# Kernel tuning notes

Measured on AMD Instinct MI355X. Metric: run time of the kernel, lower is better.

Reference implementation:

```python
import jax, jax.numpy as jnp
import numpy as np

N_NODES = 50000
N_EDGES = 800000
N_GRAPHS = 64
PIP = 3
N_CLASSES = 10
EPS = 1e-5


def setup_inputs() -> dict:
    key = jax.random.key(0)
    ks = jax.random.split(key, 32)
    s = 0.05
    d = {}
    d["node_feats"] = jax.random.normal(ks[0], (N_NODES, 128), jnp.float32)
    d["edge_w"] = jax.random.uniform(ks[1], (N_EDGES,), jnp.float32)
    # stacked per-branch params
    d["conv_w"] = jax.random.normal(ks[2], (PIP, 96, 128, 3), jnp.float32) * s
    d["conv_b"] = jax.random.normal(ks[3], (PIP, 96), jnp.float32) * s
    d["gcn_w"] = jax.random.normal(ks[4], (PIP, 96, 54), jnp.float32) * s
    d["gcn_b"] = jax.random.normal(ks[5], (PIP, 54), jnp.float32) * s
    d["bn1_g"] = jnp.ones((96,), jnp.float32)
    d["bn1_b"] = jnp.zeros((96,), jnp.float32)
    d["bn2_g"] = jnp.ones((54,), jnp.float32)
    d["bn2_b"] = jnp.zeros((54,), jnp.float32)
    d["bn3_g"] = jnp.ones((75,), jnp.float32)
    d["bn3_b"] = jnp.zeros((75,), jnp.float32)
    d["press_w"] = jax.random.normal(ks[6], (1, PIP, PIP), jnp.float32) * s
    d["press_b"] = jax.random.normal(ks[7], (1,), jnp.float32) * s
    d["jk_w1"] = jax.random.normal(ks[8], (54, 34), jnp.float32) * s
    d["jk_b1"] = jax.random.normal(ks[9], (34,), jnp.float32) * s
    d["jk_w2"] = jax.random.normal(ks[10], (34, 25), jnp.float32) * s
    d["jk_b2"] = jax.random.normal(ks[11], (25,), jnp.float32) * s
    d["jk_w3"] = jax.random.normal(ks[12], (25, 16), jnp.float32) * s
    d["jk_b3"] = jax.random.normal(ks[13], (16,), jnp.float32) * s
    d["cls1_w"] = jax.random.normal(ks[14], (75, 120), jnp.float32) * s
    d["cls1_b"] = jax.random.normal(ks[15], (120,), jnp.float32) * s
    d["cls2_w"] = jax.random.normal(ks[16], (120, N_CLASSES), jnp.float32) * s
    d["cls2_b"] = jax.random.normal(ks[17], (N_CLASSES,), jnp.float32) * s
    d["edge_src"] = jax.random.randint(ks[18], (N_EDGES,), 0, N_NODES)
    d["edge_dst"] = jax.random.randint(ks[19], (N_EDGES,), 0, N_NODES)
    d["graph_ids"] = jnp.sort(jax.random.randint(ks[20], (N_NODES,), 0, N_GRAPHS))
    return d


def _bn(x, g, b):
    # training-mode BatchNorm1d over axis 0
    m = x.mean(0)
    v = x.var(0)
    return g * (x - m) * jax.lax.rsqrt(v + EPS) + b


def _gconv(h, W, b, src, dst, ew, n):
    # DGL GraphConv norm='none': sum_{(u,v)} w_e * h[u] -> @W + b
    msg = h[src] * ew[:, None]              # [E, F]
    agg = jax.ops.segment_sum(msg, dst, num_segments=n)  # [N, F]
    return agg @ W + b


def _dconv1d(x, w, b, dil):
    # x: [1, Cin, N], w: [Cout, Cin, K]; 'same' length via pad=dil for K=3
    out = jax.lax.conv_general_dilated(
        x, w, window_strides=(1,), padding=[(dil, dil)],
        rhs_dilation=(dil,), dimension_numbers=('NCH', 'OIH', 'NCH'))
    return out + b[None, :, None]


def reference(node_feats, edge_w, conv_w, conv_b, gcn_w, gcn_b,
              bn1_g, bn1_b, bn2_g, bn2_b, bn3_g, bn3_b,
              press_w, press_b, jk_w1, jk_b1, jk_w2, jk_b2, jk_w3, jk_b3,
              cls1_w, cls1_b, cls2_w, cls2_b,
              edge_src, edge_dst, graph_ids):
    n = node_feats.shape[0]
    relu = jax.nn.relu
    # ---- BN_embedding ----
    h0 = node_feats.T[None]                # [1, 128, N]
    h0x = [_dconv1d(h0, conv_w[i], conv_b[i], i + 1) for i in range(PIP)]
    h2x = []
    for i in range(PIP):
        a = h0x[i % PIP][0].T              # [N, 96]
        c = h0x[(i + 1) % PIP][0].T        # [N, 96]
        h1 = _bn(relu(a) + c, bn1_g, bn1_b)          # cross_connect
        t = _gconv(h1, gcn_w[i], gcn_b[i], edge_src, edge_dst, edge_w, n)
        h2x.append(relu(t))                # [N, 54]
    stacked = jnp.stack(h2x, axis=1)       # [N, PIP, 54]
    pressed = jax.lax.conv_general_dilated(
        stacked, press_w, window_strides=(1,), padding='SAME',
        dimension_numbers=('NCH', 'OIH', 'NCH')) + press_b[None, :, None]
    emd_h = _bn(pressed[:, 0, :], bn2_g, bn2_b)      # [N, 54] (dropout = identity, eval)
    # ---- Presentation (JK readout) ----
    h1 = relu(_gconv(emd_h, jk_w1, jk_b1, edge_src, edge_dst, edge_w, n))
    h2 = relu(_gconv(h1, jk_w2, jk_b2, edge_src, edge_dst, edge_w, n))
    h3 = relu(_gconv(h2, jk_w3, jk_b3, edge_src, edge_dst, edge_w, n))
    ac_h = jnp.concatenate([h1, h2, h3], axis=1)     # [N, 75]
    hg = jax.ops.segment_sum(ac_h, graph_ids, num_segments=N_GRAPHS)  # [B, 75]
    logits = _bn(hg, bn3_g, bn3_b) @ cls1_w + cls1_b
    logits = logits @ cls2_w + cls2_b
    return (logits, emd_h)
```

## Files before the change

### kernel.cpp

```cpp
#include <hip/hip_runtime.h>
#include <hip/hip_bf16.h>

#define NND 50000
#define NED 800000
#define NGR 64
#define EPSV 1e-5f
#define NSTR (NND + 8)

__global__ void hist_kernel(const int* __restrict__ dst, int* __restrict__ cnt)
{
    int e = blockIdx.x * 256 + threadIdx.x;
    if (e < NED) atomicAdd(&cnt[dst[e]], 1);
}

__global__ void scanA_kernel(const int* __restrict__ cnt, int* __restrict__ bsum)
{
    __shared__ int buf[256];
    int t = threadIdx.x, base = blockIdx.x * 1024;
    int s = 0;
    for (int i = t; i < 1024; i += 256) {
        int idx = base + i;
        s += (idx < NND) ? cnt[idx] : 0;
    }
    buf[t] = s; __syncthreads();
    for (int off = 128; off; off >>= 1) {
        if (t < off) buf[t] += buf[t + off];
        __syncthreads();
    }
    if (t == 0) bsum[blockIdx.x] = buf[0];
}

__global__ void scanB_kernel(int* __restrict__ bsum, int* __restrict__ rowptr, int nb)
{
    if (threadIdx.x == 0) {
        int acc = 0;
        for (int i = 0; i < nb; i++) { int v = bsum[i]; bsum[i] = acc; acc += v; }
        rowptr[NND] = acc;
    }
}

__global__ void scanC_kernel(const int* __restrict__ cnt, const int* __restrict__ bsum,
                             int* __restrict__ rowptr, int* __restrict__ cursor)
{
    __shared__ int buf[1024];
    int t = threadIdx.x, idx = blockIdx.x * 1024 + t;
    int v = (idx < NND) ? cnt[idx] : 0;
    buf[t] = v; __syncthreads();
    for (int off = 1; off < 1024; off <<= 1) {
        int x = (t >= off) ? buf[t - off] : 0;
        __syncthreads();
        buf[t] += x;
        __syncthreads();
    }
    if (idx < NND) {
        int excl = buf[t] - v + bsum[blockIdx.x];
        rowptr[idx] = excl; cursor[idx] = excl;
    }
}

__global__ void fill_kernel(const int* __restrict__ src, const int* __restrict__ dst,
                            const float* __restrict__ ew, int* __restrict__ cursor,
                            int* __restrict__ csrs, float* __restrict__ csrw)
{
    int e = blockIdx.x * 256 + threadIdx.x;
    if (e < NED) {
        int pos = atomicAdd(&cursor[dst[e]], 1);
        csrs[pos] = src[e];
        csrw[pos] = ew[e];
    }
}

__global__ void grstart_kernel(const int* __restrict__ gid, int* __restrict__ gr)
{
    int t = threadIdx.x;
    if (t > NGR) return;
    if (t == NGR) { gr[NGR] = NND; return; }
    int lo = 0, hi = NND;
    while (lo < hi) { int mid = (lo + hi) >> 1; if (gid[mid] < t) lo = mid + 1; else hi = mid; }
    gr[t] = lo;
}

__global__ void transpose_kernel(const float* __restrict__ nf, float* __restrict__ nfT)
{
    __shared__ float tile[32][33];
    int tx = threadIdx.x & 31, ty = threadIdx.x >> 5;
    int p0 = blockIdx.x * 32, c0 = blockIdx.y * 32;
#pragma unroll
    for (int i = 0; i < 4; i++) {
        int p = p0 + ty + i * 8;
        if (p < NND) tile[ty + i * 8][tx] = nf[(size_t)p * 128 + c0 + tx];
    }
    __syncthreads();
#pragma unroll
    for (int i = 0; i < 4; i++) {
        int c = c0 + ty + i * 8;
        int p = p0 + tx;
        if (p < NND) nfT[(size_t)c * NSTR + 4 + p] = tile[tx][ty + i * 8];
    }
}

__global__ void pad_kernel(float* __restrict__ nfT)
{
    int t = threadIdx.x;
    int c = t >> 3, i = t & 7;
    size_t off = (size_t)c * NSTR + (i < 4 ? i : (NND + i));
    nfT[off] = 0.f;
}

template <int D>
__device__ __forceinline__ void conv_body(const float* __restrict__ nfT,
                                          const float* __restrict__ wl,
                                          const int pq0, const int pq1,
                                          float acc[2][8][4])
{
    for (int c = 0; c < 128; c++) {
        const float* col = nfT + (size_t)c * NSTR + 4;
        float4 lo[2], mi[2], hi[2];
        lo[0] = *(const float4*)(col + pq0 - 4);
        mi[0] = *(const float4*)(col + pq0);
        hi[0] = *(const float4*)(col + pq0 + 4);
        lo[1] = *(const float4*)(col + pq1 - 4);
        mi[1] = *(const float4*)(col + pq1);
        hi[1] = *(const float4*)(col + pq1 + 4);
        float f0[2][4], f1[2][4], f2[2][4];
#pragma unroll
        for (int q = 0; q < 2; q++) {
            f1[q][0] = mi[q].x; f1[q][1] = mi[q].y; f1[q][2] = mi[q].z; f1[q][3] = mi[q].w;
            if (D == 1) {
                f0[q][0] = lo[q].w; f0[q][1] = mi[q].x; f0[q][2] = mi[q].y; f0[q][3] = mi[q].z;
                f2[q][0] = mi[q].y; f2[q][1] = mi[q].z; f2[q][2] = mi[q].w; f2[q][3] = hi[q].x;
            } else if (D == 2) {
                f0[q][0] = lo[q].z; f0[q][1] = lo[q].w; f0[q][2] = mi[q].x; f0[q][3] = mi[q].y;
                f2[q][0] = mi[q].z; f2[q][1] = mi[q].w; f2[q][2] = hi[q].x; f2[q][3] = hi[q].y;
            } else {
                f0[q][0] = lo[q].y; f0[q][1] = lo[q].z; f0[q][2] = lo[q].w; f0[q][3] = mi[q].x;
                f2[q][0] = mi[q].w; f2[q][1] = hi[q].x; f2[q][2] = hi[q].y; f2[q][3] = hi[q].z;
            }
        }
        const float4* w0 = (const float4*)&wl[(0 * 128 + c) * 8];
        const float4* w1 = (const float4*)&wl[(1 * 128 + c) * 8];
        const float4* w2 = (const float4*)&wl[(2 * 128 + c) * 8];
#pragma unroll
        for (int jh = 0; jh < 2; jh++) {
            float4 a0 = w0[jh], a1 = w1[jh], a2 = w2[jh];
#pragma unroll
            for (int q = 0; q < 2; q++)
#pragma unroll
                for (int i = 0; i < 4; i++) {
                    acc[q][jh * 4 + 0][i] += f0[q][i] * a0.x + f1[q][i] * a1.x + f2[q][i] * a2.x;
                    acc[q][jh * 4 + 1][i] += f0[q][i] * a0.y + f1[q][i] * a1.y + f2[q][i] * a2.y;
                    acc[q][jh * 4 + 2][i] += f0[q][i] * a0.z + f1[q][i] * a1.z + f2[q][i] * a2.z;
                    acc[q][jh * 4 + 3][i] += f0[q][i] * a0.w + f1[q][i] * a1.w + f2[q][i] * a2.w;
                }
        }
    }
}

__global__ __launch_bounds__(256, 3)
void conv_kernel(const float* __restrict__ nfT, const float* __restrict__ cw,
                 const float* __restrict__ cb, float* __restrict__ X)
{
    __shared__ __align__(16) float wl[3 * 128 * 8];
    const int t  = threadIdx.x;
    const int og = blockIdx.y;
    const int br = blockIdx.z;
    for (int l = t; l < 3 * 128 * 8; l += 256) {
        int j = l & 7; int c = (l >> 3) & 127; int k = l >> 10;
        wl[l] = cw[(((size_t)br * 96 + og * 8 + j) * 128 + c) * 3 + k];
    }
    __syncthreads();
    const int pq0 = blockIdx.x * 2048 + t * 4;
    const int pq1 = pq0 + 1024;
    float acc[2][8][4];
#pragma unroll
    for (int j = 0; j < 8; j++) {
        float b = cb[br * 96 + og * 8 + j];
#pragma unroll
        for (int q = 0; q < 2; q++)
#pragma unroll
            for (int i = 0; i < 4; i++) acc[q][j][i] = b;
    }
    if (br == 0)      conv_body<1>(nfT, wl, pq0, pq1, acc);
    else if (br == 1) conv_body<2>(nfT, wl, pq0, pq1, acc);
    else              conv_body<3>(nfT, wl, pq0, pq1, acc);
#pragma unroll
    for (int q = 0; q < 2; q++) {
        int pb = q ? pq1 : pq0;
#pragma unroll
        for (int i = 0; i < 4; i++) {
            int p = pb + i;
            if (p >= NND) continue;
            float* xo = X + (size_t)br * NND * 96 + (size_t)p * 96 + og * 8;
            float4 v0, v1;
            v0.x = acc[q][0][i]; v0.y = acc[q][1][i]; v0.z = acc[q][2][i]; v0.w = acc[q][3][i];
            v1.x = acc[q][4][i]; v1.y = acc[q][5][i]; v1.z = acc[q][6][i]; v1.w = acc[q][7][i];
            ((float4*)xo)[0] = v0;
            ((float4*)xo)[1] = v1;
        }
    }
}

__global__ void y_stats_kernel(const float* __restrict__ X, float* __restrict__ Y,
                               float* __restrict__ st1)
{
    __shared__ float ls[384], lq[384];
    int t = threadIdx.x;
    int br = blockIdx.y, ip1 = (br + 1) % 3;
    int c = t % 96, rsub = t / 96;
    const size_t NM = (size_t)NND * 96;
    int r0 = blockIdx.x * 64;
    int rend = r0 + 64 < NND ? r0 + 64 : NND;
    float s = 0.f, q = 0.f;
    const float* Xa = X + (size_t)br * NM;
    const float* Xb = X + (size_t)ip1 * NM;
    float* Yb = Y + (size_t)br * NM;
    for (int r = r0 + rsub; r < rend; r += 4) {
        size_t idx = (size_t)r * 96 + c;
        float a = Xa[idx]; a = a > 0.f ? a : 0.f;
        float y = a + Xb[idx];
        Yb[idx] = y;
        s += y; q += y * y;
    }
    ls[t] = s; lq[t] = q;
    __syncthreads();
    if (t < 96) {
        s = ls[t] + ls[t + 96] + ls[t + 192] + ls[t + 288];
        q = lq[t] + lq[t + 96] + lq[t + 192] + lq[t + 288];
        unsafeAtomicAdd(&st1[br * 96 + t], s);
        unsafeAtomicAdd(&st1[288 + br * 96 + t], q);
    }
}

__global__ void bn_finalize_kernel(const float* __restrict__ st, const float* __restrict__ g,
                                   const float* __restrict__ b,
                                   float* __restrict__ sc, float* __restrict__ sh,
                                   int C, int gmod)
{
    int t = threadIdx.x;
    if (t >= C) return;
    float mean = st[t] / (float)NND;
    float var  = st[C + t] / (float)NND - mean * mean;
    float rs = rsqrtf(var + EPSV);
    float gg = g[t % gmod], bb = b[t % gmod];
    float s = gg * rs;
    sc[t] = s; sh[t] = bb - mean * s;
}

__global__ void pull_bn_kernel(const float* __restrict__ Y, const int* __restrict__ rowptr,
                               const int* __restrict__ csrs, const float* __restrict__ csrw,
                               const float* __restrict__ sc1, const float* __restrict__ sh1,
                               float* __restrict__ AGG)
{
    int id = blockIdx.x * 256 + threadIdx.x;
    if (id >= NND * 24) return;
    int p = id / 24, q = id % 24;
    const float4* Y4 = (const float4*)Y;
    const size_t NQ = (size_t)NND * 24;
    int beg = rowptr[p], end = rowptr[p + 1];
    float a0x=0,a0y=0,a0z=0,a0w=0, a1x=0,a1y=0,a1z=0,a1w=0, a2x=0,a2y=0,a2z=0,a2w=0;
    float wsum = 0.f;
    for (int i = beg; i < end; i++) {
        float w = csrw[i];
        size_t off = (size_t)csrs[i] * 24 + q;
        float4 v0 = Y4[off];
        float4 v1 = Y4[NQ + off];
        float4 v2 = Y4[2 * NQ + off];
        a0x += w * v0.x; a0y += w * v0.y; a0z += w * v0.z; a0w += w * v0.w;
        a1x += w * v1.x; a1y += w * v1.y; a1z += w * v1.z; a1w += w * v1.w;
        a2x += w * v2.x; a2y += w * v2.y; a2z += w * v2.z; a2w += w * v2.w;
        wsum += w;
    }
    const float4* S4 = (const float4*)sc1;
    const float4* H4 = (const float4*)sh1;
    float4* AG4 = (float4*)AGG;
    size_t ob = (size_t)p * 24 + q;
    {
        float4 s = S4[q], h = H4[q], r;
        r.x = s.x * a0x + h.x * wsum; r.y = s.y * a0y + h.y * wsum;
        r.z = s.z * a0z + h.z * wsum; r.w = s.w * a0w + h.w * wsum;
        AG4[ob] = r;
    }
    {
        float4 s = S4[24 + q], h = H4[24 + q], r;
        r.x = s.x * a1x + h.x * wsum; r.y = s.y * a1y + h.y * wsum;
        r.z = s.z * a1z + h.z * wsum; r.w = s.w * a1w + h.w * wsum;
        AG4[NQ + ob] = r;
    }
    {
        float4 s = S4[48 + q], h = H4[48 + q], r;
        r.x = s.x * a2x + h.x * wsum; r.y = s.y * a2y + h.y * wsum;
        r.z = s.z * a2z + h.z * wsum; r.w = s.w * a2w + h.w * wsum;
        AG4[2 * NQ + ob] = r;
    }
}

template <int C>
__global__ void pull2_kernel(const float* __restrict__ in, const int* __restrict__ rowptr,
                             const int* __restrict__ csrs, const float* __restrict__ csrw,
                             float* __restrict__ out)
{
    constexpr int C2 = C / 2;
    int id = blockIdx.x * 256 + threadIdx.x;
    if (id >= NND * C2) return;
    int p = id / C2, q = id % C2;
    const float2* in2 = (const float2*)in;
    int beg = rowptr[p], end = rowptr[p + 1];
    float ax = 0.f, ay = 0.f;
    for (int i = beg; i < end; i++) {
        float w = csrw[i];
        float2 v = in2[(size_t)csrs[i] * C2 + q];
        ax += w * v.x; ay += w * v.y;
    }
    float2 r; r.x = ax; r.y = ay;
    ((float2*)out)[(size_t)p * C2 + q] = r;
}

template <int C>
__global__ void pull_kernel(const float* __restrict__ in, const int* __restrict__ rowptr,
                            const int* __restrict__ csrs, const float* __restrict__ csrw,
                            float* __restrict__ out)
{
    int id = blockIdx.x * 256 + threadIdx.x;
    if (id >= NND * C) return;
    int p = id / C, c = id % C;
    int beg = rowptr[p], end = rowptr[p + 1];
    float acc = 0.f;
    for (int i = beg; i < end; i++)
        acc += csrw[i] * in[(size_t)csrs[i] * C + c];
    out[id] = acc;
}

template <int Cin, int Cout>
__global__ __launch_bounds__(128)
void matmul_node_kernel(const float* __restrict__ in, const float* __restrict__ W,
                        const float* __restrict__ bias, float* __restrict__ out)
{
    constexpr int CoutP = (Cout + 3) & ~3;
    __shared__ __align__(16) float wl[Cin * CoutP];
    __shared__ float bl[CoutP];
    const int t = threadIdx.x;
    const int br = blockIdx.y;
    const float* Wb = W + (size_t)br * Cin * Cout;
    for (int l = t; l < Cin * CoutP; l += 128) {
        int c = l / CoutP, o = l % CoutP;
        wl[l] = (o < Cout) ? Wb[c * Cout + o] : 0.f;
    }
    if (t < CoutP) bl[t] = (t < Cout) ? bias[br * Cout + t] : 0.f;
    __syncthreads();
    int p = blockIdx.x * 128 + t;
    if (p >= NND) return;
    float acc[CoutP];
#pragma unroll
    for (int o = 0; o < CoutP; o++) acc[o] = bl[o];
    const float* row = in + (size_t)br * NND * Cin + (size_t)p * Cin;
    if constexpr (Cin % 4 == 0) {
        const float4* row4 = (const float4*)row;
#pragma unroll
        for (int c4 = 0; c4 < Cin / 4; c4++) {
            float4 f4 = row4[c4];
            float fv[4] = {f4.x, f4.y, f4.z, f4.w};
#pragma unroll
            for (int cc = 0; cc < 4; cc++) {
                const float4* w4 = (const float4*)&wl[(c4 * 4 + cc) * CoutP];
#pragma unroll
                for (int oq = 0; oq < CoutP / 4; oq++) {
                    float4 wv = w4[oq];
                    acc[oq * 4 + 0] += fv[cc] * wv.x;
                    acc[oq * 4 + 1] += fv[cc] * wv.y;
                    acc[oq * 4 + 2] += fv[cc] * wv.z;
                    acc[oq * 4 + 3] += fv[cc] * wv.w;
                }
            }
        }
    } else if constexpr (Cin % 2 == 0) {
        const float2* row2 = (const float2*)row;
#pragma unroll
        for (int c2 = 0; c2 < Cin / 2; c2++) {
            float2 f2 = row2[c2];
            float fv[2] = {f2.x, f2.y};
#pragma unroll
            for (int cc = 0; cc < 2; cc++) {
                const float4* w4 = (const float4*)&wl[(c2 * 2 + cc) * CoutP];
#pragma unroll
                for (int oq = 0; oq < CoutP / 4; oq++) {
                    float4 wv = w4[oq];
                    acc[oq * 4 + 0] += fv[cc] * wv.x;
                    acc[oq * 4 + 1] += fv[cc] * wv.y;
                    acc[oq * 4 + 2] += fv[cc] * wv.z;
                    acc[oq * 4 + 3] += fv[cc] * wv.w;
                }
            }
        }
    } else {
#pragma unroll
        for (int c = 0; c < Cin; c++) {
            float f = row[c];
            const float4* w4 = (const float4*)&wl[c * CoutP];
#pragma unroll
            for (int oq = 0; oq < CoutP / 4; oq++) {
                float4 wv = w4[oq];
                acc[oq * 4 + 0] += f * wv.x;
                acc[oq * 4 + 1] += f * wv.y;
                acc[oq * 4 + 2] += f * wv.z;
                acc[oq * 4 + 3] += f * wv.w;
            }
        }
    }
    float* op = out + (size_t)br * NND * Cout + (size_t)p * Cout;
    if constexpr (Cout % 2 == 0) {
#pragma unroll
        for (int o2 = 0; o2 < Cout / 2; o2++) {
            float2 r;
            r.x = acc[o2 * 2] > 0.f ? acc[o2 * 2] : 0.f;
            r.y = acc[o2 * 2 + 1] > 0.f ? acc[o2 * 2 + 1] : 0.f;
            ((float2*)op)[o2] = r;
        }
    } else {
#pragma unroll
        for (int o = 0; o < Cout; o++) op[o] = acc[o] > 0.f ? acc[o] : 0.f;
    }
}

__global__ void press_stats_kernel(const float* __restrict__ H2, const float* __restrict__ pw,
                                   const float* __restrict__ pb, float* __restrict__ PRS,
                                   float* __restrict__ st2)
{
    __shared__ float ls[54], lq[54];
    int t = threadIdx.x;
    if (t < 54) { ls[t] = 0.f; lq[t] = 0.f; }
    __syncthreads();
    float pwf[9];
#pragma unroll
    for (int q = 0; q < 9; q++) pwf[q] = pw[q];
    float pbf = pb[0];
    const size_t NM = (size_t)NND * 54;
    size_t base = (size_t)blockIdx.x * 6912;
    for (int q = 0; q < 27; q++) {
        size_t idx = base + q * 256 + t;
        if (idx < NM) {
            int p = (int)(idx / 54), h = (int)(idx % 54);
            float sum = pbf;
#pragma unroll
            for (int i = 0; i < 3; i++)
#pragma unroll
                for (int k = 0; k < 3; k++) {
                    int hh = h + k - 1;
                    if (hh >= 0 && hh < 54)
                        sum += pwf[i * 3 + k] * H2[(size_t)i * NM + (size_t)p * 54 + hh];
                }
            PRS[idx] = sum;
            atomicAdd(&ls[h], sum); atomicAdd(&lq[h], sum * sum);
        }
    }
    __syncthreads();
    if (t < 54) {
        unsafeAtomicAdd(&st2[t], ls[t]);
        unsafeAtomicAdd(&st2[54 + t], lq[t]);
    }
}

__global__ void emd_kernel(float* __restrict__ PRS, const float* __restrict__ sc2,
                           const float* __restrict__ sh2, float* __restrict__ outp)
{
    int id = blockIdx.x * 256 + threadIdx.x;
    if (id >= NND * 54) return;
    int h = id % 54;
    float v = PRS[id] * sc2[h] + sh2[h];
    PRS[id] = v;
    outp[id] = v;
}

__global__ void pool_kernel(const float* __restrict__ H1, const float* __restrict__ H2j,
                            const float* __restrict__ H3, const int* __restrict__ gr,
                            float* __restrict__ HG)
{
    __shared__ float part[4][75];
    int t = threadIdx.x;
    int c = t % 75, sub = t / 75;
    int g = blockIdx.x;
    int s = gr[g], e = gr[g + 1];
    float acc = 0.f;
    for (int p = s + sub; p < e; p += 4) {
        float v;
        if (c < 34)      v = H1[(size_t)p * 34 + c];
        else if (c < 59) v = H2j[(size_t)p * 25 + (c - 34)];
        else             v = H3[(size_t)p * 16 + (c - 59)];
        acc += v;
    }
    part[sub][c] = acc;
    __syncthreads();
    if (t < 75) HG[g * 75 + t] = part[0][t] + part[1][t] + part[2][t] + part[3][t];
}

__global__ void final_kernel(const float* __restrict__ HG, const float* __restrict__ g3,
                             const float* __restrict__ b3,
                             const float* __restrict__ w1, const float* __restrict__ b1,
                             const float* __restrict__ w2, const float* __restrict__ b2,
                             float* __restrict__ outp)
{
    __shared__ float hg[64 * 75];
    __shared__ float o1[64 * 120];
    __shared__ float sc[75], sh[75];
    int t = threadIdx.x;
    for (int idx = t; idx < 64 * 75; idx += 512) hg[idx] = HG[idx];
    __syncthreads();
    if (t < 75) {
        float s = 0.f, q = 0.f;
        for (int r = 0; r < 64; r++) { float v = hg[r * 75 + t]; s += v; q += v * v; }
        float m = s / 64.f, var = q / 64.f - m * m;
        float rs = rsqrtf(var + EPSV);
        float scale = g3[t] * rs;
        sc[t] = scale; sh[t] = b3[t] - m * scale;
    }
    __syncthreads();
    for (int idx = t; idx < 64 * 75; idx += 512) { int c = idx % 75; hg[idx] = hg[idx] * sc[c] + sh[c]; }
    __syncthreads();
    for (int idx = t; idx < 64 * 120; idx += 512) {
        int r = idx / 120, o = idx % 120;
        float a = b1[o];
        for (int c = 0; c < 75; c++) a += hg[r * 75 + c] * w1[c * 120 + o];
        o1[idx] = a;
    }
    __syncthreads();
    for (int idx = t; idx < 640; idx += 512) {
        int r = idx / 10, o = idx % 10;
        float a = b2[o];
        for (int k = 0; k < 120; k++) a += o1[r * 120 + k] * w2[k * 10 + o];
        outp[idx] = a;
    }
}

extern "C" void kernel_launch(void* const* d_in, const int* in_sizes, int n_in,
                              void* d_out, int out_size, void* d_ws, size_t ws_size,
                              hipStream_t stream)
{
    (void)in_sizes; (void)n_in; (void)out_size;
    const float* nf     = (const float*)d_in[0];
    const float* ew     = (const float*)d_in[1];
    const float* conv_w = (const float*)d_in[2];
    const float* conv_b = (const float*)d_in[3];
    const float* gcn_w  = (const float*)d_in[4];
    const float* gcn_b  = (const float*)d_in[5];
    const float* bn1_g = (const float*)d_in[6],  *bn1_b = (const float*)d_in[7];
    const float* bn2_g = (const float*)d_in[8],  *bn2_b = (const float*)d_in[9];
    const float* bn3_g = (const float*)d_in[10], *bn3_b = (const float*)d_in[11];
    const float* press_w = (const float*)d_in[12], *press_b = (const float*)d_in[13];
    const float* jk_w1 = (const float*)d_in[14], *jk_b1 = (const float*)d_in[15];
    const float* jk_w2 = (const float*)d_in[16], *jk_b2 = (const float*)d_in[17];
    const float* jk_w3 = (const float*)d_in[18], *jk_b3 = (const float*)d_in[19];
    const float* cls1_w = (const float*)d_in[20], *cls1_b = (const float*)d_in[21];
    const float* cls2_w = (const float*)d_in[22], *cls2_b = (const float*)d_in[23];
    const int* esrc = (const int*)d_in[24];
    const int* edst = (const int*)d_in[25];
    const int* gid  = (const int*)d_in[26];
    float* out = (float*)d_out;

    float* ws = (float*)d_ws;
    const size_t NM = (size_t)NND * 96;
    const size_t N54 = (size_t)NND * 54;
    float* X   = ws;
    float* Y   = X + 3 * NM;
    float* H2c = Y + 3 * NM;
    float* PRS = H2c + 3 * N54;
    float* ST1 = PRS + N54;
    float* SC1 = ST1 + 576;
    float* SH1 = SC1 + 288;
    float* ST2 = SH1 + 288;
    float* SC2 = ST2 + 108;
    float* SH2 = SC2 + 54;
    float* HG  = SH2 + 54;
    int* CNT    = (int*)(HG + 4800);
    int* ROWPTR = CNT + NND;
    int* CURSOR = ROWPTR + NND + 1;
    int* CSRS   = CURSOR + NND;
    float* CSRW = (float*)(CSRS + NED);
    int* BSUM   = (int*)(CSRW + NED);
    int* GR     = BSUM + 64;
    size_t need = (size_t)((float*)(GR + 65) - ws) * sizeof(float);
    if (ws_size < need) return;

    float* nfT  = Y;
    float* AGG  = X;
    float* AGG1 = Y;
    float* H1j  = AGG1 + N54;
    float* AGG2 = H1j + (size_t)NND * 34;
    float* H2j  = AGG2 + (size_t)NND * 34;
    float* AGG3 = H2j + (size_t)NND * 25;
    float* H3j  = AGG3 + (size_t)NND * 25;

    hipMemsetAsync(ST1, 0, 1368 * sizeof(float), stream);
    hipMemsetAsync(CNT, 0, NND * sizeof(int), stream);

    hist_kernel<<<(NED + 255) / 256, 256, 0, stream>>>(edst, CNT);
    scanA_kernel<<<49, 256, 0, stream>>>(CNT, BSUM);
    scanB_kernel<<<1, 64, 0, stream>>>(BSUM, ROWPTR, 49);
    scanC_kernel<<<49, 1024, 0, stream>>>(CNT, BSUM, ROWPTR, CURSOR);
    fill_kernel<<<(NED + 255) / 256, 256, 0, stream>>>(esrc, edst, ew, CURSOR, CSRS, CSRW);
    grstart_kernel<<<1, 128, 0, stream>>>(gid, GR);

    transpose_kernel<<<dim3((NND + 31) / 32, 4), 256, 0, stream>>>(nf, nfT);
    pad_kernel<<<1, 1024, 0, stream>>>(nfT);

    conv_kernel<<<dim3(25, 12, 3), 256, 0, stream>>>(nfT, conv_w, conv_b, X);

    y_stats_kernel<<<dim3((NND + 63) / 64, 3), 384, 0, stream>>>(X, Y, ST1);
    bn_finalize_kernel<<<1, 512, 0, stream>>>(ST1, bn1_g, bn1_b, SC1, SH1, 288, 96);

    pull_bn_kernel<<<(NND * 24 + 255) / 256, 256, 0, stream>>>(
        Y, ROWPTR, CSRS, CSRW, SC1, SH1, AGG);

    matmul_node_kernel<96, 54><<<dim3((NND + 127) / 128, 3), 128, 0, stream>>>(
        AGG, gcn_w, gcn_b, H2c);

    press_stats_kernel<<<(int)((N54 + 6911) / 6912), 256, 0, stream>>>(H2c, press_w, press_b, PRS, ST2);
    bn_finalize_kernel<<<1, 512, 0, stream>>>(ST2, bn2_g, bn2_b, SC2, SH2, 54, 54);
    emd_kernel<<<(int)((N54 + 255) / 256), 256, 0, stream>>>(PRS, SC2, SH2, out + 640);

    pull2_kernel<54><<<(NND * 27 + 255) / 256, 256, 0, stream>>>(PRS, ROWPTR, CSRS, CSRW, AGG1);
    matmul_node_kernel<54, 34><<<dim3((NND + 127) / 128, 1), 128, 0, stream>>>(
        AGG1, jk_w1, jk_b1, H1j);

    pull2_kernel<34><<<(NND * 17 + 255) / 256, 256, 0, stream>>>(H1j, ROWPTR, CSRS, CSRW, AGG2);
    matmul_node_kernel<34, 25><<<dim3((NND + 127) / 128, 1), 128, 0, stream>>>(
        AGG2, jk_w2, jk_b2, H2j);

    pull_kernel<25><<<(NND * 25 + 255) / 256, 256, 0, stream>>>(H2j, ROWPTR, CSRS, CSRW, AGG3);
    matmul_node_kernel<25, 16><<<dim3((NND + 127) / 128, 1), 128, 0, stream>>>(
        AGG3, jk_w3, jk_b3, H3j);

    pool_kernel<<<NGR, 300, 0, stream>>>(H1j, H2j, H3j, GR, HG);
    final_kernel<<<1, 512, 0, stream>>>(HG, bn3_g, bn3_b, cls1_w, cls1_b, cls2_w, cls2_b, out);
}
```

Measured before the change: 1.020 ms.

## Fuse three-branch conv with cross-connect and BN statistics in one kernel

Each block now computes all three dilated conv branches for the same output-channel group and node tile. The input column loads are shared across branches, and the relu(a)+c cross-connect and the BN sum/sumsq reduction (wave shuffles plus atomics) are applied in registers. This removes the separate y_stats pass and the round trip of the intermediate X buffer through global memory. In exchange the accumulator count grows to 96 registers per thread and the launch_bounds occupancy hint is dropped, so occupancy may fall. The transposed input now lives in the X buffer so that Y can be written directly.

```diff
diff --git a/kernel.cpp b/kernel.cpp
--- a/kernel.cpp
+++ b/kernel.cpp
@@ -108,127 +108,115 @@
 }
 
 template <int D>
-__device__ __forceinline__ void conv_body(const float* __restrict__ nfT,
-                                          const float* __restrict__ wl,
-                                          const int pq0, const int pq1,
-                                          float acc[2][8][4])
-{
+__device__ __forceinline__ void conv_tap(const float4& lo, const float4& mi, const float4& hi,
+                                         const float* __restrict__ wl, int c,
+                                         float (&acc)[8][4])
+{
+    float f0[4], f1[4], f2[4];
+    f1[0] = mi.x; f1[1] = mi.y; f1[2] = mi.z; f1[3] = mi.w;
+    if (D == 1) {
+        f0[0] = lo.w; f0[1] = mi.x; f0[2] = mi.y; f0[3] = mi.z;
+        f2[0] = mi.y; f2[1] = mi.z; f2[2] = mi.w; f2[3] = hi.x;
+    } else if (D == 2) {
+        f0[0] = lo.z; f0[1] = lo.w; f0[2] = mi.x; f0[3] = mi.y;
+        f2[0] = mi.z; f2[1] = mi.w; f2[2] = hi.x; f2[3] = hi.y;
+    } else {
+        f0[0] = lo.y; f0[1] = lo.z; f0[2] = lo.w; f0[3] = mi.x;
+        f2[0] = mi.w; f2[1] = hi.x; f2[2] = hi.y; f2[3] = hi.z;
+    }
+    const int BR = D - 1;
+    const float4* w0 = (const float4*)&wl[((BR * 3 + 0) * 128 + c) * 8];
+    const float4* w1 = (const float4*)&wl[((BR * 3 + 1) * 128 + c) * 8];
+    const float4* w2 = (const float4*)&wl[((BR * 3 + 2) * 128 + c) * 8];
+#pragma unroll
+    for (int jh = 0; jh < 2; jh++) {
+        float4 a0 = w0[jh], a1 = w1[jh], a2 = w2[jh];
+#pragma unroll
+        for (int i = 0; i < 4; i++) {
+            acc[jh * 4 + 0][i] += f0[i] * a0.x + f1[i] * a1.x + f2[i] * a2.x;
+            acc[jh * 4 + 1][i] += f0[i] * a0.y + f1[i] * a1.y + f2[i] * a2.y;
+            acc[jh * 4 + 2][i] += f0[i] * a0.z + f1[i] * a1.z + f2[i] * a2.z;
+            acc[jh * 4 + 3][i] += f0[i] * a0.w + f1[i] * a1.w + f2[i] * a2.w;
+        }
+    }
+}
+
+__global__ __launch_bounds__(256)
+void conv_y_stats_kernel(const float* __restrict__ nfT, const float* __restrict__ cw,
+                         const float* __restrict__ cb, float* __restrict__ Y,
+                         float* __restrict__ st1)
+{
+    __shared__ __align__(16) float wl[3 * 3 * 128 * 8];
+    const int t  = threadIdx.x;
+    const int og = blockIdx.x;
+    for (int l = t; l < 3 * 3 * 128 * 8; l += 256) {
+        int j = l & 7; int c = (l >> 3) & 127; int kb = l >> 10;
+        int k = kb % 3, br = kb / 3;
+        wl[l] = cw[(((size_t)br * 96 + og * 8 + j) * 128 + c) * 3 + k];
+    }
+    __syncthreads();
+    const int pq = blockIdx.y * 1024 + t * 4;
+    float acc[3][8][4];
+#pragma unroll
+    for (int br = 0; br < 3; br++) {
+#pragma unroll
+        for (int j = 0; j < 8; j++) {
+            float b = cb[br * 96 + og * 8 + j];
+#pragma unroll
+            for (int i = 0; i < 4; i++) acc[br][j][i] = b;
+        }
+    }
     for (int c = 0; c < 128; c++) {
         const float* col = nfT + (size_t)c * NSTR + 4;
-        float4 lo[2], mi[2], hi[2];
-        lo[0] = *(const float4*)(col + pq0 - 4);
-        mi[0] = *(const float4*)(col + pq0);
-        hi[0] = *(const float4*)(col + pq0 + 4);
-        lo[1] = *(const float4*)(col + pq1 - 4);
-        mi[1] = *(const float4*)(col + pq1);
-        hi[1] = *(const float4*)(col + pq1 + 4);
-        float f0[2][4], f1[2][4], f2[2][4];
-#pragma unroll
-        for (int q = 0; q < 2; q++) {
-            f1[q][0] = mi[q].x; f1[q][1] = mi[q].y; f1[q][2] = mi[q].z; f1[q][3] = mi[q].w;
-            if (D == 1) {
-                f0[q][0] = lo[q].w; f0[q][1] = mi[q].x; f0[q][2] = mi[q].y; f0[q][3] = mi[q].z;
-                f2[q][0] = mi[q].y; f2[q][1] = mi[q].z; f2[q][2] = mi[q].w; f2[q][3] = hi[q].x;
-            } else if (D == 2) {
-                f0[q][0] = lo[q].z; f0[q][1] = lo[q].w; f0[q][2] = mi[q].x; f0[q][3] = mi[q].y;
-                f2[q][0] = mi[q].z; f2[q][1] = mi[q].w; f2[q][2] = hi[q].x; f2[q][3] = hi[q].y;
-            } else {
-                f0[q][0] = lo[q].y; f0[q][1] = lo[q].z; f0[q][2] = lo[q].w; f0[q][3] = mi[q].x;
-                f2[q][0] = mi[q].w; f2[q][1] = hi[q].x; f2[q][2] = hi[q].y; f2[q][3] = hi[q].z;
+        float4 lo = *(const float4*)(col + pq - 4);
+        float4 mi = *(const float4*)(col + pq);
+        float4 hi = *(const float4*)(col + pq + 4);
+        conv_tap<1>(lo, mi, hi, wl, c, acc[0]);
+        conv_tap<2>(lo, mi, hi, wl, c, acc[1]);
+        conv_tap<3>(lo, mi, hi, wl, c, acc[2]);
+    }
+#pragma unroll
+    for (int j = 0; j < 8; j++)
+#pragma unroll
+        for (int i = 0; i < 4; i++) {
+            float a0 = acc[0][j][i], a1 = acc[1][j][i], a2 = acc[2][j][i];
+            acc[0][j][i] = (a0 > 0.f ? a0 : 0.f) + a1;
+            acc[1][j][i] = (a1 > 0.f ? a1 : 0.f) + a2;
+            acc[2][j][i] = (a2 > 0.f ? a2 : 0.f) + a0;
+        }
+    bool val[4];
+#pragma unroll
+    for (int i = 0; i < 4; i++) val[i] = (pq + i) < NND;
+    const size_t NM = (size_t)NND * 96;
+#pragma unroll
+    for (int br = 0; br < 3; br++)
+#pragma unroll
+        for (int j = 0; j < 8; j++) {
+            float s = 0.f, q = 0.f;
+#pragma unroll
+            for (int i = 0; i < 4; i++)
+                if (val[i]) { float v = acc[br][j][i]; s += v; q += v * v; }
+            for (int off = 32; off; off >>= 1) {
+                s += __shfl_down(s, off, 64);
+                q += __shfl_down(q, off, 64);
             }
-        }
-        const float4* w0 = (const float4*)&wl[(0 * 128 + c) * 8];
-        const float4* w1 = (const float4*)&wl[(1 * 128 + c) * 8];
-        const float4* w2 = (const float4*)&wl[(2 * 128 + c) * 8];
-#pragma unroll
-        for (int jh = 0; jh < 2; jh++) {
-            float4 a0 = w0[jh], a1 = w1[jh], a2 = w2[jh];
-#pragma unroll
-            for (int q = 0; q < 2; q++)
-#pragma unroll
-                for (int i = 0; i < 4; i++) {
-                    acc[q][jh * 4 + 0][i] += f0[q][i] * a0.x + f1[q][i] * a1.x + f2[q][i] * a2.x;
-                    acc[q][jh * 4 + 1][i] += f0[q][i] * a0.y + f1[q][i] * a1.y + f2[q][i] * a2.y;
-                    acc[q][jh * 4 + 2][i] += f0[q][i] * a0.z + f1[q][i] * a1.z + f2[q][i] * a2.z;
-                    acc[q][jh * 4 + 3][i] += f0[q][i] * a0.w + f1[q][i] * a1.w + f2[q][i] * a2.w;
-                }
-        }
-    }
-}
-
-__global__ __launch_bounds__(256, 3)
-void conv_kernel(const float* __restrict__ nfT, const float* __restrict__ cw,
-                 const float* __restrict__ cb, float* __restrict__ X)
-{
-    __shared__ __align__(16) float wl[3 * 128 * 8];
-    const int t  = threadIdx.x;
-    const int og = blockIdx.y;
-    const int br = blockIdx.z;
-    for (int l = t; l < 3 * 128 * 8; l += 256) {
-        int j = l & 7; int c = (l >> 3) & 127; int k = l >> 10;
-        wl[l] = cw[(((size_t)br * 96 + og * 8 + j) * 128 + c) * 3 + k];
-    }
-    __syncthreads();
-    const int pq0 = blockIdx.x * 2048 + t * 4;
-    const int pq1 = pq0 + 1024;
-    float acc[2][8][4];
-#pragma unroll
-    for (int j = 0; j < 8; j++) {
-        float b = cb[br * 96 + og * 8 + j];
-#pragma unroll
-        for (int q = 0; q < 2; q++)
-#pragma unroll
-            for (int i = 0; i < 4; i++) acc[q][j][i] = b;
-    }
-    if (br == 0)      conv_body<1>(nfT, wl, pq0, pq1, acc);
-    else if (br == 1) conv_body<2>(nfT, wl, pq0, pq1, acc);
-    else              conv_body<3>(nfT, wl, pq0, pq1, acc);
-#pragma unroll
-    for (int q = 0; q < 2; q++) {
-        int pb = q ? pq1 : pq0;
+            if ((t & 63) == 0) {
+                unsafeAtomicAdd(&st1[br * 96 + og * 8 + j], s);
+                unsafeAtomicAdd(&st1[288 + br * 96 + og * 8 + j], q);
+            }
+        }
+#pragma unroll
+    for (int br = 0; br < 3; br++)
 #pragma unroll
         for (int i = 0; i < 4; i++) {
-            int p = pb + i;
-            if (p >= NND) continue;
-            float* xo = X + (size_t)br * NND * 96 + (size_t)p * 96 + og * 8;
+            if (!val[i]) continue;
+            float* yo = Y + (size_t)br * NM + (size_t)(pq + i) * 96 + og * 8;
             float4 v0, v1;
-            v0.x = acc[q][0][i]; v0.y = acc[q][1][i]; v0.z = acc[q][2][i]; v0.w = acc[q][3][i];
-            v1.x = acc[q][4][i]; v1.y = acc[q][5][i]; v1.z = acc[q][6][i]; v1.w = acc[q][7][i];
-            ((float4*)xo)[0] = v0;
-            ((float4*)xo)[1] = v1;
-        }
-    }
-}
-
-__global__ void y_stats_kernel(const float* __restrict__ X, float* __restrict__ Y,
-                               float* __restrict__ st1)
-{
-    __shared__ float ls[384], lq[384];
-    int t = threadIdx.x;
-    int br = blockIdx.y, ip1 = (br + 1) % 3;
-    int c = t % 96, rsub = t / 96;
-    const size_t NM = (size_t)NND * 96;
-    int r0 = blockIdx.x * 64;
-    int rend = r0 + 64 < NND ? r0 + 64 : NND;
-    float s = 0.f, q = 0.f;
-    const float* Xa = X + (size_t)br * NM;
-    const float* Xb = X + (size_t)ip1 * NM;
-    float* Yb = Y + (size_t)br * NM;
-    for (int r = r0 + rsub; r < rend; r += 4) {
-        size_t idx = (size_t)r * 96 + c;
-        float a = Xa[idx]; a = a > 0.f ? a : 0.f;
-        float y = a + Xb[idx];
-        Yb[idx] = y;
-        s += y; q += y * y;
-    }
-    ls[t] = s; lq[t] = q;
-    __syncthreads();
-    if (t < 96) {
-        s = ls[t] + ls[t + 96] + ls[t + 192] + ls[t + 288];
-        q = lq[t] + lq[t + 96] + lq[t + 192] + lq[t + 288];
-        unsafeAtomicAdd(&st1[br * 96 + t], s);
-        unsafeAtomicAdd(&st1[288 + br * 96 + t], q);
-    }
+            v0.x = acc[br][0][i]; v0.y = acc[br][1][i]; v0.z = acc[br][2][i]; v0.w = acc[br][3][i];
+            v1.x = acc[br][4][i]; v1.y = acc[br][5][i]; v1.z = acc[br][6][i]; v1.w = acc[br][7][i];
+            ((float4*)yo)[0] = v0;
+            ((float4*)yo)[1] = v1;
+        }
 }
 
 __global__ void bn_finalize_kernel(const float* __restrict__ st, const float* __restrict__ g,
@@ -579,7 +567,7 @@
     size_t need = (size_t)((float*)(GR + 65) - ws) * sizeof(float);
     if (ws_size < need) return;
 
-    float* nfT  = Y;
+    float* nfT  = X;
     float* AGG  = X;
     float* AGG1 = Y;
     float* H1j  = AGG1 + N54;
@@ -601,9 +589,7 @@
     transpose_kernel<<<dim3((NND + 31) / 32, 4), 256, 0, stream>>>(nf, nfT);
     pad_kernel<<<1, 1024, 0, stream>>>(nfT);
 
-    conv_kernel<<<dim3(25, 12, 3), 256, 0, stream>>>(nfT, conv_w, conv_b, X);
-
-    y_stats_kernel<<<dim3((NND + 63) / 64, 3), 384, 0, stream>>>(X, Y, ST1);
+    conv_y_stats_kernel<<<dim3(12, 49), 256, 0, stream>>>(nfT, conv_w, conv_b, Y, ST1);
     bn_finalize_kernel<<<1, 512, 0, stream>>>(ST1, bn1_g, bn1_b, SC1, SH1, 288, 96);
 
     pull_bn_kernel<<<(NND * 24 + 255) / 256, 256, 0, stream>>>(
```

Measured after the change: 1.036 ms. No clear change (+1.5%).
